# Kernel optimization log

Measured on AMD Instinct MI355X. Metric: run time of the kernel, lower is better.

The kernel has to match this reference:

```python
import jax, jax.numpy as jnp
import numpy as np

B, S = 16, 8192
Q_DIM, K_DIM, ATTN_DIM = 512, 512, 512


def setup_inputs() -> dict:
    key = jax.random.key(0)
    k1, k2, k3, k4, k5, k6 = jax.random.split(key, 6)
    query = jax.random.normal(k1, (B, Q_DIM), dtype=jnp.float32)
    keys = jax.random.normal(k2, (B, S, K_DIM), dtype=jnp.float32)
    mask = jax.random.randint(k3, (B, S), 0, 2, dtype=jnp.int32)
    # learned params (torch Linear stores weight as [out, in]; we keep [in, out])
    Wq = jax.random.normal(k4, (Q_DIM, ATTN_DIM), dtype=jnp.float32) / np.sqrt(Q_DIM)
    Wk = jax.random.normal(k5, (K_DIM, ATTN_DIM), dtype=jnp.float32) / np.sqrt(K_DIM)
    v = jax.random.normal(k6, (ATTN_DIM,), dtype=jnp.float32) / np.sqrt(ATTN_DIM)
    return {"query": query, "keys": keys, "mask": mask, "Wq": Wq, "Wk": Wk, "v": v}


def reference(query, keys, mask, Wq, Wk, v):
    # q: [B, 1, A], k: [B, S, A]
    q = (query @ Wq)[:, None, :]
    k = jnp.einsum('bsk,ka->bsa', keys, Wk)
    # scores e: [B, S]  (v-projection reduces attn dim)
    e = jnp.einsum('bsa,a->bs', jnp.tanh(q + k), v)
    neg_min = jnp.finfo(e.dtype).min
    e = jnp.where(mask == 0, neg_min, e)
    a = jax.nn.softmax(e, axis=-1)  # [B, S]
    c = jnp.einsum('bs,bsk->bk', a, keys)  # context [B, K_DIM]
    return (c, a)
```

## Files before the change

### kernel.cpp

```cpp
#include <hip/hip_runtime.h>

#define BB 16
#define SS 8192
#define DD 512

typedef float  f32x4  __attribute__((ext_vector_type(4)));
typedef __bf16 bf16x8 __attribute__((ext_vector_type(8)));
typedef __bf16 bf16x4 __attribute__((ext_vector_type(4)));

__device__ __forceinline__ void cvt_store_bf4(unsigned short* dst, f32x4 v) {
    bf16x4 o;
    o.x = (__bf16)v.x; o.y = (__bf16)v.y; o.z = (__bf16)v.z; o.w = (__bf16)v.w;
    *(bf16x4*)dst = o;
}

__device__ __forceinline__ float tanh_fast(float x) {
    float e2 = __expf(2.0f * x);
    return 1.0f - 2.0f / (e2 + 1.0f);
}

__device__ __forceinline__ void bar_lgkm() {
    asm volatile("s_waitcnt lgkmcnt(0)\n\ts_barrier" ::: "memory");
}

__global__ __launch_bounds__(256) void prep_kernel(
    const float* __restrict__ query, const float* __restrict__ Wq,
    const float* __restrict__ Wk, float* __restrict__ qproj,
    unsigned short* __restrict__ WkT_f)
{
    __shared__ __bf16 lt[64][65];
    const int bid = blockIdx.x, t = threadIdx.x;
    if (bid < 64) {
        const int k0 = (bid >> 3) * 64, n0 = (bid & 7) * 64;
#pragma unroll
        for (int rep = 0; rep < 4; ++rep) {
            const int k = rep * 16 + (t >> 4), n = (t & 15) * 4;
            f32x4 vv = *(const f32x4*)&Wk[(size_t)(k0 + k) * DD + n0 + n];
            lt[k][n] = (__bf16)vv.x; lt[k][n + 1] = (__bf16)vv.y;
            lt[k][n + 2] = (__bf16)vv.z; lt[k][n + 3] = (__bf16)vv.w;
        }
        __syncthreads();
        const int g_loc = t >> 6, lane = t & 63;
        const int ml = lane & 15, quad = lane >> 4;
        const int g = (bid & 7) * 4 + g_loc;
#pragma unroll
        for (int j_loc = 0; j_loc < 2; ++j_loc) {
            const int j = (bid >> 3) * 2 + j_loc;
            bf16x8 o;
#pragma unroll
            for (int d = 0; d < 8; ++d)
                o[d] = lt[j_loc * 32 + quad * 8 + d][g_loc * 16 + ml];
            *(bf16x8*)&WkT_f[((size_t)((g * 16 + j) * 64 + lane)) * 8] = o;
        }
    } else {
        const int idx = (bid - 64) * 256 + t;
        const int b = idx >> 9;
        const int n = idx & 511;
        const float* q  = query + b * DD;
        const float* wp = Wq + n;
        float acc = 0.0f;
#pragma unroll 8
        for (int k = 0; k < DD; ++k)
            acc = fmaf(q[k], wp[(size_t)k * DD], acc);
        qproj[b * DD + n] = acc;
    }
}

__global__ __launch_bounds__(512, 2) void fused_kernel(
    const float* __restrict__ keys, const unsigned short* __restrict__ WkT_f,
    const float* __restrict__ qproj, const float* __restrict__ vvec,
    const int* __restrict__ mask, float* __restrict__ e_ws,
    float* __restrict__ cpart, float2* __restrict__ ml_ws)
{
    __shared__ unsigned short ksA[2][16 * 2048];
    __shared__ float sm_part[8][64];
    __shared__ float w_sh[64];
    __shared__ f32x4 red[3][128];

    const int tid  = threadIdx.x;
    const int w    = tid >> 6;
    const int lane = tid & 63;
    const int ml   = lane & 15;
    const int quad = lane >> 4;
    const int bid  = blockIdx.x;
    const int b    = bid >> 4;
    const int c0   = (bid & 15) << 3;

    const int m  = tid >> 3;
    const int q8 = tid & 7;
    const int it = m >> 4;
    const int sq = q8 >> 1;
    const int j0 = (q8 & 1) * 4;
    const int base = it * 512 + ((m & 15) + 16 * sq) * 8 + j0;
    const float* krow0 = keys + ((size_t)(b * SS + c0 * 64 + m)) * DD + q8 * 4;

    const unsigned short* wfb = WkT_f + (size_t)w * 32768 + lane * 8;

    const int l   = tid & 127;
    const int sh  = tid >> 7;
    const int n4  = l << 2;
    const int cbase = (l >> 3) * 2048 + sh * 512 + ((l >> 1) & 3) * 128 + (l & 1) * 4;
    const int rot   = (l & 15) + (l >> 3);

    float qv[4], vv[4];
#pragma unroll
    for (int jn = 0; jn < 4; ++jn) {
        const int n = w * 64 + jn * 16 + ml;
        qv[jn] = qproj[b * DD + n];
        vv[jn] = vvec[n];
    }

    {
        f32x4 kst[8];
#pragma unroll
        for (int h = 0; h < 2; ++h) {
#pragma unroll
            for (int j = 0; j < 8; ++j)
                kst[j] = __builtin_nontemporal_load(
                             (const f32x4*)(krow0 + (h * 8 + j) * 32));
#pragma unroll
            for (int j = 0; j < 8; ++j)
                cvt_store_bf4(&ksA[0][(h * 8 + j) * 2048 + base], kst[j]);
        }
    }
    bar_lgkm();

#pragma unroll 1
    for (int t = 0; t < 8; ++t) {
        const int ping = t & 1;
        const int c  = c0 + t;
        const int s0 = c << 6;
        const unsigned short* ksp = ksA[ping];

        f32x4 kst[16];
        if (t < 7) {
            const float* knext = krow0 + (size_t)(t + 1) * 32768;
#pragma unroll
            for (int j = 0; j < 16; ++j)
                kst[j] = __builtin_nontemporal_load(
                             (const f32x4*)(knext + j * 32));
        }

        int mk = 0;
        if (tid < 64) mk = mask[(size_t)b * SS + s0 + tid];

        f32x4 acc[4][4];
#pragma unroll
        for (int i = 0; i < 4; ++i)
#pragma unroll
            for (int jn = 0; jn < 4; ++jn) acc[i][jn] = (f32x4){0.f, 0.f, 0.f, 0.f};

#pragma unroll 4
        for (int j = 0; j < 16; ++j) {
            bf16x8 af[4];
#pragma unroll
            for (int i = 0; i < 4; ++i)
                af[i] = *(const bf16x8*)&ksp[j * 2048 + (i * 64 + lane) * 8];
#pragma unroll
            for (int jn = 0; jn < 4; ++jn) {
                bf16x8 bfr = *(const bf16x8*)(wfb + ((jn * 16 + j) << 9));
#pragma unroll
                for (int i = 0; i < 4; ++i)
                    acc[i][jn] = __builtin_amdgcn_mfma_f32_16x16x32_bf16(af[i], bfr, acc[i][jn], 0, 0, 0);
            }
        }

#pragma unroll
        for (int i = 0; i < 4; ++i) {
#pragma unroll
            for (int r = 0; r < 4; ++r) {
                float s = 0.0f;
#pragma unroll
                for (int jn = 0; jn < 4; ++jn) {
                    float xx = acc[i][jn][r] + qv[jn];
                    s += tanh_fast(xx) * vv[jn];
                }
                s += __shfl_xor(s, 1, 64);
                s += __shfl_xor(s, 2, 64);
                s += __shfl_xor(s, 4, 64);
                s += __shfl_xor(s, 8, 64);
                if (ml == 0) sm_part[w][i * 16 + quad * 4 + r] = s;
            }
        }
        bar_lgkm();

        if (tid < 64) {
            float e = sm_part[0][tid] + sm_part[1][tid] + sm_part[2][tid] + sm_part[3][tid]
                    + sm_part[4][tid] + sm_part[5][tid] + sm_part[6][tid] + sm_part[7][tid];
            if (mk == 0) e = -3.402823466e38f;
            e_ws[(size_t)b * SS + s0 + tid] = e;
            float mx = e;
#pragma unroll
            for (int off = 32; off >= 1; off >>= 1) mx = fmaxf(mx, __shfl_xor(mx, off, 64));
            float wv = (mk == 0) ? 0.0f : __expf(e - mx);
            float lsum = wv;
#pragma unroll
            for (int off = 32; off >= 1; off >>= 1) lsum += __shfl_xor(lsum, off, 64);
            w_sh[tid] = wv;
            if (tid == 0) ml_ws[b * 128 + c] = make_float2(mx, lsum);
        }
        bar_lgkm();

        if (t < 7) {
#pragma unroll
            for (int j = 0; j < 16; ++j)
                cvt_store_bf4(&ksA[ping ^ 1][j * 2048 + base], kst[j]);
        }

        f32x4 cacc = (f32x4){0.f, 0.f, 0.f, 0.f};
#pragma unroll
        for (int p = 0; p < 16; ++p) {
            const int sI = (p + rot) & 15;
            bf16x4 kv = *(const bf16x4*)&ksp[cbase + sI * 8];
            const float wgt = w_sh[sh * 16 + sI];
            cacc.x += wgt * (float)kv.x;
            cacc.y += wgt * (float)kv.y;
            cacc.z += wgt * (float)kv.z;
            cacc.w += wgt * (float)kv.w;
        }
        if (sh) red[sh - 1][l] = cacc;
        bar_lgkm();

        if (sh == 0) {
            cacc += red[0][l] + red[1][l] + red[2][l];
            *(f32x4*)(cpart + ((size_t)(b * 128 + c)) * 512 + n4) = cacc;
        }
    }
}

__global__ __launch_bounds__(256) void finalize_kernel(
    const float* __restrict__ e_ws, const float* __restrict__ cpart,
    const float2* __restrict__ ml_ws, float* __restrict__ out)
{
    __shared__ float rm[4], rs[4];
    __shared__ float sc_sh[128];
    __shared__ float cred[4][512];
    const int bid = blockIdx.x, t = threadIdx.x;
    const int b = (bid < 16) ? bid : ((bid - 16) >> 3);

    float mi = -3.402823466e38f, li = 0.0f;
    if (t < 128) { float2 p = ml_ws[b * 128 + t]; mi = p.x; li = p.y; }
    float mr = mi;
#pragma unroll
    for (int off = 32; off >= 1; off >>= 1) mr = fmaxf(mr, __shfl_xor(mr, off, 64));
    if ((t & 63) == 0) rm[t >> 6] = mr;
    __syncthreads();
    const float M = fmaxf(fmaxf(rm[0], rm[1]), fmaxf(rm[2], rm[3]));
    float si = (t < 128) ? li * __expf(mi - M) : 0.0f;
#pragma unroll
    for (int off = 32; off >= 1; off >>= 1) si += __shfl_xor(si, off, 64);
    if ((t & 63) == 0) rs[t >> 6] = si;
    __syncthreads();
    const float L = rs[0] + rs[1] + rs[2] + rs[3];
    const float invL = 1.0f / L;

    if (bid < 16) {
        if (t < 128) sc_sh[t] = __expf(ml_ws[b * 128 + t].x - M);
        __syncthreads();
        const int w2 = t >> 6, l = t & 63;
        float pa[8] = {0.f, 0.f, 0.f, 0.f, 0.f, 0.f, 0.f, 0.f};
#pragma unroll 4
        for (int i = w2 * 32; i < w2 * 32 + 32; ++i) {
            const float sc = sc_sh[i];
            const float* cp = cpart + ((size_t)(b * 128 + i)) * 512 + l * 8;
#pragma unroll
            for (int c = 0; c < 8; ++c) pa[c] = fmaf(cp[c], sc, pa[c]);
        }
#pragma unroll
        for (int c = 0; c < 8; ++c) cred[w2][l * 8 + c] = pa[c];
        __syncthreads();
#pragma unroll
        for (int rep = 0; rep < 2; ++rep) {
            const int n = t + rep * 256;
            out[b * DD + n] = (cred[0][n] + cred[1][n] + cred[2][n] + cred[3][n]) * invL;
        }
    } else {
        const int chunk8 = (bid - 16) & 7;
        const float* ep = e_ws + (size_t)b * SS + chunk8 * 1024;
        float* ap = out + BB * DD + (size_t)b * SS + chunk8 * 1024;
#pragma unroll
        for (int r = 0; r < 4; ++r) {
            float e = ep[t + 256 * r];
            ap[t + 256 * r] = __expf(e - M) * invL;
        }
    }
}

extern "C" void kernel_launch(void* const* d_in, const int* in_sizes, int n_in,
                              void* d_out, int out_size, void* d_ws, size_t ws_size,
                              hipStream_t stream)
{
    const float* query = (const float*)d_in[0];
    const float* keys  = (const float*)d_in[1];
    const int*   mask  = (const int*)  d_in[2];
    const float* Wq    = (const float*)d_in[3];
    const float* Wk    = (const float*)d_in[4];
    const float* v     = (const float*)d_in[5];
    float* out = (float*)d_out;

    float*          qproj = (float*)d_ws;
    unsigned short* WkT_f = (unsigned short*)((char*)d_ws + 32768);
    float*          e_ws  = (float*)((char*)d_ws + 32768 + 524288);
    float*          cpart = (float*)((char*)d_ws + 32768 + 2 * 524288);
    float2*         ml_ws = (float2*)((char*)d_ws + 32768 + 2 * 524288 + 4194304);

    prep_kernel    <<<96, 256, 0, stream>>>(query, Wq, Wk, qproj, WkT_f);
    fused_kernel   <<<256, 512, 0, stream>>>(keys, WkT_f, qproj, v, mask,
                                             e_ws, cpart, ml_ws);
    finalize_kernel<<<16 + 128, 256, 0, stream>>>(e_ws, cpart, ml_ws, out);
}
```

Measured before the change: 483.9 us.

## Software-pipeline chunk loop: overlap tanh epilogue of previous chunk with current MFMAs

Restructures the per-chunk loop so the tanh/v-projection epilogue of chunk t-1 is interleaved segment-by-segment with the MFMA k-loop of chunk t, using two ping-pong accumulator sets. The global prefetch of the next key chunk is moved to the last MFMA segment, and the context accumulation for the previous chunk runs after. The aim is to hide transcendental ALU latency and global-load latency behind matrix-core work. It doubles the accumulator register footprint (another 64 VGPRs), which may cause spilling or reduce occupancy under launch_bounds(512,2), and it adds a prologue and epilogue stage.

```diff
diff --git a/kernel.cpp b/kernel.cpp
--- a/kernel.cpp
+++ b/kernel.cpp
@@ -66,13 +66,69 @@
     }
 }
 
+template<bool EPI, bool KST>
+__device__ __forceinline__ void chunk_kloop(
+    f32x4 (&acc)[4][4], const f32x4 (&prv)[4][4],
+    const unsigned short* __restrict__ ksp,
+    const unsigned short* __restrict__ wfb,
+    const float (&qv)[4], const float (&vv)[4],
+    float* __restrict__ sm_slot, const int ml, const int lane,
+    f32x4 (&kst)[16], const float* __restrict__ knext)
+{
+#pragma unroll
+    for (int i = 0; i < 4; ++i)
+#pragma unroll
+        for (int jn = 0; jn < 4; ++jn) acc[i][jn] = (f32x4){0.f, 0.f, 0.f, 0.f};
+
+#pragma unroll
+    for (int seg = 0; seg < 4; ++seg) {
+        if (KST && seg == 3) {
+#pragma unroll
+            for (int j2 = 0; j2 < 16; ++j2)
+                kst[j2] = __builtin_nontemporal_load(
+                              (const f32x4*)(knext + j2 * 32));
+        }
+#pragma unroll
+        for (int jj = 0; jj < 4; ++jj) {
+            const int j = seg * 4 + jj;
+            bf16x8 af[4];
+#pragma unroll
+            for (int i = 0; i < 4; ++i)
+                af[i] = *(const bf16x8*)&ksp[j * 2048 + (i * 64 + lane) * 8];
+#pragma unroll
+            for (int jn = 0; jn < 4; ++jn) {
+                bf16x8 bfr = *(const bf16x8*)(wfb + ((jn * 16 + j) << 9));
+#pragma unroll
+                for (int i = 0; i < 4; ++i)
+                    acc[i][jn] = __builtin_amdgcn_mfma_f32_16x16x32_bf16(af[i], bfr, acc[i][jn], 0, 0, 0);
+            }
+        }
+        if (EPI) {
+            const int i = seg;
+#pragma unroll
+            for (int r = 0; r < 4; ++r) {
+                float s = 0.0f;
+#pragma unroll
+                for (int jn = 0; jn < 4; ++jn)
+                    s += tanh_fast(prv[i][jn][r] + qv[jn]) * vv[jn];
+                s += __shfl_xor(s, 1, 64);
+                s += __shfl_xor(s, 2, 64);
+                s += __shfl_xor(s, 4, 64);
+                s += __shfl_xor(s, 8, 64);
+                if (ml == 0) sm_slot[i * 16 + r] = s;
+            }
+        }
+    }
+}
+
 __global__ __launch_bounds__(512, 2) void fused_kernel(
     const float* __restrict__ keys, const unsigned short* __restrict__ WkT_f,
     const float* __restrict__ qproj, const float* __restrict__ vvec,
     const int* __restrict__ mask, float* __restrict__ e_ws,
     float* __restrict__ cpart, float2* __restrict__ ml_ws)
 {
-    __shared__ unsigned short ksA[2][16 * 2048];
+    __shared__ unsigned short buf0[16 * 2048];
+    __shared__ unsigned short buf1[16 * 2048];
     __shared__ float sm_part[8][64];
     __shared__ float w_sh[64];
     __shared__ f32x4 red[3][128];
@@ -88,10 +144,7 @@
 
     const int m  = tid >> 3;
     const int q8 = tid & 7;
-    const int it = m >> 4;
-    const int sq = q8 >> 1;
-    const int j0 = (q8 & 1) * 4;
-    const int base = it * 512 + ((m & 15) + 16 * sq) * 8 + j0;
+    const int base = (m >> 4) * 512 + ((m & 15) + 16 * (q8 >> 1)) * 8 + (q8 & 1) * 4;
     const float* krow0 = keys + ((size_t)(b * SS + c0 * 64 + m)) * DD + q8 * 4;
 
     const unsigned short* wfb = WkT_f + (size_t)w * 32768 + lane * 8;
@@ -109,109 +162,140 @@
         qv[jn] = qproj[b * DD + n];
         vv[jn] = vvec[n];
     }
+    float* sm_slot = &sm_part[w][quad * 4];
+
+    f32x4 accA[4][4], accB[4][4];
+    f32x4 kst[16];
+    int mk_prev = 0;
+    if (tid < 64) mk_prev = mask[(size_t)b * SS + (c0 << 6) + tid];
 
     {
-        f32x4 kst[8];
+        f32x4 st[8];
 #pragma unroll
         for (int h = 0; h < 2; ++h) {
 #pragma unroll
             for (int j = 0; j < 8; ++j)
-                kst[j] = __builtin_nontemporal_load(
-                             (const f32x4*)(krow0 + (h * 8 + j) * 32));
+                st[j] = __builtin_nontemporal_load(
+                            (const f32x4*)(krow0 + (h * 8 + j) * 32));
 #pragma unroll
             for (int j = 0; j < 8; ++j)
-                cvt_store_bf4(&ksA[0][(h * 8 + j) * 2048 + base], kst[j]);
+                cvt_store_bf4(&buf0[(h * 8 + j) * 2048 + base], st[j]);
         }
     }
     bar_lgkm();
 
+    chunk_kloop<false, true>(accA, accB, buf0, wfb, qv, vv, sm_slot, ml, lane,
+                             kst, krow0 + 32768);
+#pragma unroll
+    for (int j2 = 0; j2 < 16; ++j2)
+        cvt_store_bf4(&buf1[j2 * 2048 + base], kst[j2]);
+    bar_lgkm();
+
+#define CHUNK_BODY(CUR, PRV, T, BUFC, BUFO, KSTF)                              \
+    {                                                                          \
+        const int c_prev = c0 + (T) - 1;                                       \
+        const int s0p = c_prev << 6;                                           \
+        int mk_next = 0;                                                       \
+        if (tid < 64) mk_next = mask[(size_t)b * SS + ((c0 + (T)) << 6) + tid];\
+        chunk_kloop<true, KSTF>(CUR, PRV, BUFC, wfb, qv, vv, sm_slot, ml,      \
+                                lane, kst, krow0 + (size_t)((T) + 1) * 32768); \
+        bar_lgkm();                                         \
+        if (tid < 64) {                                                        \
+            float e = sm_part[0][tid] + sm_part[1][tid] + sm_part[2][tid]      \
+                    + sm_part[3][tid] + sm_part[4][tid] + sm_part[5][tid]      \
+                    + sm_part[6][tid] + sm_part[7][tid];                       \
+            if (mk_prev == 0) e = -3.402823466e38f;                            \
+            e_ws[(size_t)b * SS + s0p + tid] = e;                              \
+            float mx = e;                                                      \
+            _Pragma("unroll")                                                  \
+            for (int off = 32; off >= 1; off >>= 1)                            \
+                mx = fmaxf(mx, __shfl_xor(mx, off, 64));                       \
+            float wv = (mk_prev == 0) ? 0.0f : __expf(e - mx);                 \
+            float lsum = wv;                                                   \
+            _Pragma("unroll")                                                  \
+            for (int off = 32; off >= 1; off >>= 1)                            \
+                lsum += __shfl_xor(lsum, off, 64);                             \
+            w_sh[tid] = wv;                                                    \
+            if (tid == 0) ml_ws[b * 128 + c_prev] = make_float2(mx, lsum);     \
+        }                                                                      \
+        mk_prev = mk_next;                                                     \
+        bar_lgkm();                                            \
+        f32x4 cacc = (f32x4){0.f, 0.f, 0.f, 0.f};                              \
+        _Pragma("unroll")                                                      \
+        for (int p = 0; p < 16; ++p) {                                         \
+            const int sI = (p + rot) & 15;                                     \
+            bf16x4 kv = *(const bf16x4*)&BUFO[cbase + sI * 8];                 \
+            const float wgt = w_sh[sh * 16 + sI];                              \
+            cacc.x += wgt * (float)kv.x;                                       \
+            cacc.y += wgt * (float)kv.y;                                       \
+            cacc.z += wgt * (float)kv.z;                                       \
+            cacc.w += wgt * (float)kv.w;                                       \
+        }                                                                      \
+        if (sh) red[sh - 1][l] = cacc;                                         \
+        bar_lgkm();                            \
+        if (sh == 0) {                                                         \
+            cacc += red[0][l] + red[1][l] + red[2][l];                         \
+            *(f32x4*)(cpart + ((size_t)(b * 128 + c_prev)) * 512 + n4) = cacc; \
+        }                                                                      \
+        if (KSTF) {                                                            \
+            _Pragma("unroll")                                                  \
+            for (int j2 = 0; j2 < 16; ++j2)                                    \
+                cvt_store_bf4(&BUFO[j2 * 2048 + base], kst[j2]);               \
+        }                                                                      \
+        bar_lgkm();                                   \
+    }
+
 #pragma unroll 1
-    for (int t = 0; t < 8; ++t) {
-        const int ping = t & 1;
-        const int c  = c0 + t;
+    for (int tp = 0; tp < 3; ++tp) {
+        CHUNK_BODY(accB, accA, 2 * tp + 1, buf1, buf0, true);
+        CHUNK_BODY(accA, accB, 2 * tp + 2, buf0, buf1, true);
+    }
+    CHUNK_BODY(accB, accA, 7, buf1, buf0, false);
+#undef CHUNK_BODY
+
+    {
+        const int c = c0 + 7;
         const int s0 = c << 6;
-        const unsigned short* ksp = ksA[ping];
-
-        f32x4 kst[16];
-        if (t < 7) {
-            const float* knext = krow0 + (size_t)(t + 1) * 32768;
-#pragma unroll
-            for (int j = 0; j < 16; ++j)
-                kst[j] = __builtin_nontemporal_load(
-                             (const f32x4*)(knext + j * 32));
-        }
-
-        int mk = 0;
-        if (tid < 64) mk = mask[(size_t)b * SS + s0 + tid];
-
-        f32x4 acc[4][4];
-#pragma unroll
-        for (int i = 0; i < 4; ++i)
-#pragma unroll
-            for (int jn = 0; jn < 4; ++jn) acc[i][jn] = (f32x4){0.f, 0.f, 0.f, 0.f};
-
-#pragma unroll 4
-        for (int j = 0; j < 16; ++j) {
-            bf16x8 af[4];
-#pragma unroll
-            for (int i = 0; i < 4; ++i)
-                af[i] = *(const bf16x8*)&ksp[j * 2048 + (i * 64 + lane) * 8];
-#pragma unroll
-            for (int jn = 0; jn < 4; ++jn) {
-                bf16x8 bfr = *(const bf16x8*)(wfb + ((jn * 16 + j) << 9));
-#pragma unroll
-                for (int i = 0; i < 4; ++i)
-                    acc[i][jn] = __builtin_amdgcn_mfma_f32_16x16x32_bf16(af[i], bfr, acc[i][jn], 0, 0, 0);
-            }
-        }
-
 #pragma unroll
         for (int i = 0; i < 4; ++i) {
 #pragma unroll
             for (int r = 0; r < 4; ++r) {
                 float s = 0.0f;
 #pragma unroll
-                for (int jn = 0; jn < 4; ++jn) {
-                    float xx = acc[i][jn][r] + qv[jn];
-                    s += tanh_fast(xx) * vv[jn];
-                }
+                for (int jn = 0; jn < 4; ++jn)
+                    s += tanh_fast(accB[i][jn][r] + qv[jn]) * vv[jn];
                 s += __shfl_xor(s, 1, 64);
                 s += __shfl_xor(s, 2, 64);
                 s += __shfl_xor(s, 4, 64);
                 s += __shfl_xor(s, 8, 64);
-                if (ml == 0) sm_part[w][i * 16 + quad * 4 + r] = s;
+                if (ml == 0) sm_slot[i * 16 + r] = s;
             }
         }
         bar_lgkm();
-
         if (tid < 64) {
-            float e = sm_part[0][tid] + sm_part[1][tid] + sm_part[2][tid] + sm_part[3][tid]
-                    + sm_part[4][tid] + sm_part[5][tid] + sm_part[6][tid] + sm_part[7][tid];
-            if (mk == 0) e = -3.402823466e38f;
+            float e = sm_part[0][tid] + sm_part[1][tid] + sm_part[2][tid]
+                    + sm_part[3][tid] + sm_part[4][tid] + sm_part[5][tid]
+                    + sm_part[6][tid] + sm_part[7][tid];
+            if (mk_prev == 0) e = -3.402823466e38f;
             e_ws[(size_t)b * SS + s0 + tid] = e;
             float mx = e;
 #pragma unroll
-            for (int off = 32; off >= 1; off >>= 1) mx = fmaxf(mx, __shfl_xor(mx, off, 64));
-            float wv = (mk == 0) ? 0.0f : __expf(e - mx);
+            for (int off = 32; off >= 1; off >>= 1)
+                mx = fmaxf(mx, __shfl_xor(mx, off, 64));
+            float wv = (mk_prev == 0) ? 0.0f : __expf(e - mx);
             float lsum = wv;
 #pragma unroll
-            for (int off = 32; off >= 1; off >>= 1) lsum += __shfl_xor(lsum, off, 64);
+            for (int off = 32; off >= 1; off >>= 1)
+                lsum += __shfl_xor(lsum, off, 64);
             w_sh[tid] = wv;
             if (tid == 0) ml_ws[b * 128 + c] = make_float2(mx, lsum);
         }
         bar_lgkm();
-
-        if (t < 7) {
-#pragma unroll
-            for (int j = 0; j < 16; ++j)
-                cvt_store_bf4(&ksA[ping ^ 1][j * 2048 + base], kst[j]);
-        }
-
         f32x4 cacc = (f32x4){0.f, 0.f, 0.f, 0.f};
 #pragma unroll
         for (int p = 0; p < 16; ++p) {
             const int sI = (p + rot) & 15;
-            bf16x4 kv = *(const bf16x4*)&ksp[cbase + sI * 8];
+            bf16x4 kv = *(const bf16x4*)&buf1[cbase + sI * 8];
             const float wgt = w_sh[sh * 16 + sI];
             cacc.x += wgt * (float)kv.x;
             cacc.y += wgt * (float)kv.y;
@@ -220,7 +304,6 @@
         }
         if (sh) red[sh - 1][l] = cacc;
         bar_lgkm();
-
         if (sh == 0) {
             cacc += red[0][l] + red[1][l] + red[2][l];
             *(f32x4*)(cpart + ((size_t)(b * 128 + c)) * 512 + n4) = cacc;
```

Measured after the change: 696.7 us. +44.0%, slower.
